# Optimization experiments

Hardware: AMD Instinct MI355X
Metric: run time of the kernel (lower is better)

## Reference

```python
import jax, jax.numpy as jnp
import numpy as np


def _cost_volume(x, y, maxdisp):
    # x, y: [N, C, H, W] left/right feature maps.
    # Replicates the torch loop:
    #   for i in range(D): d = D-1-i
    #     cost[:, :C, d, :, i:W]  = x[:, :, :, i:W]
    #     cost[:, C:, d, :, i:]   = y_pad[:, :, :, :W+D-i]   (y zero-padded to W+D)
    # =>  cost_x[d, j] = x[..., j]      if D-1-d <= j < W   else 0
    #     cost_y[d, j] = y[..., j-(D-1-d)] if 0 <= j-(D-1-d) < W else 0
    N, C, H, W = x.shape
    D = maxdisp
    Wc = W + D
    d = jnp.arange(D)
    i = (D - 1) - d                      # shift per depth plane, [D]
    j = jnp.arange(Wc)                   # output width coords, [Wc]

    # left-image half: same columns, masked per depth plane
    xp = jnp.pad(x, ((0, 0), (0, 0), (0, 0), (0, D)))          # [N,C,H,Wc]
    mask_x = (j[None, :] >= i[:, None]) & (j[None, :] < W)      # [D,Wc]
    cost_x = xp[:, :, None, :, :] * mask_x[None, None, :, None, :].astype(x.dtype)

    # right-image half: shifted gather with zero fill
    jy = j[None, :] - i[:, None]                                # [D,Wc]
    valid = (jy >= 0) & (jy < W)
    idx = jnp.clip(jy, 0, W - 1)
    y_g = y[:, :, :, idx]                                       # [N,C,H,D,Wc]
    cost_y = jnp.where(valid[None, None, None, :, :], y_g, jnp.zeros((), x.dtype))
    cost_y = cost_y.transpose(0, 1, 3, 2, 4)                    # [N,C,D,H,Wc]

    return jnp.concatenate([cost_x, cost_y], axis=1)            # [N,2C,D,H,Wc]


def setup_inputs() -> dict:
    key = jax.random.key(0)
    k1, k2 = jax.random.split(key)
    N, C, H, W = 2, 32, 64, 128
    x = jax.random.normal(k1, (N, C, H, W), dtype=jnp.float32)
    y = jax.random.normal(k2, (N, C, H, W), dtype=jnp.float32)
    return {"x": x, "y": y, "maxdisp": 48}


def reference(x, y, maxdisp):
    return _cost_volume(x, y, maxdisp)
```

## Files before the change

kernel.cpp:

```cpp
#include <hip/hip_runtime.h>

constexpr int N    = 2;
constexpr int C    = 32;
constexpr int H    = 64;
constexpr int W    = 128;
constexpr int D    = 48;
constexpr int Wc   = W + D;
constexpr int C2   = 2 * C;
constexpr int HWc  = H * Wc;
constexpr int Wc4  = Wc / 4;
constexpr int BQ   = D * Wc4;
constexpr int NBLOCKS = N * C2 * H;

typedef float vf4 __attribute__((ext_vector_type(4)));

__global__ __launch_bounds__(256)
void cost_volume_kernel(const float* __restrict__ x,
                        const float* __restrict__ y,
                        float* __restrict__ out)
{
    __shared__ __align__(16) float row[224];

    unsigned b   = blockIdx.x;
    unsigned tid = threadIdx.x;

    unsigned h  = b % H;
    unsigned t  = b / H;
    unsigned cc = t % C2;
    unsigned n  = t / C2;
    bool is_x = cc < C;

    if (is_x) {
        if (tid < 128)
            row[tid] = x[((n * C + cc) * H + h) * W + tid];
        else if (tid < 224)
            row[tid] = 0.0f;
    } else {
        if (tid < 48)
            row[tid] = 0.0f;
        else if (tid < 176)
            row[tid] = y[((n * C + (cc - C)) * H + h) * W + (tid - 48)];
        else if (tid < 224)
            row[tid] = 0.0f;
    }
    __syncthreads();

    vf4* __restrict__ outv = reinterpret_cast<vf4*>(out)
                           + (size_t)t * (D * (HWc / 4)) + h * Wc4;
    const vf4* __restrict__ rowv = reinterpret_cast<const vf4*>(row);

    if (is_x) {
        #pragma unroll
        for (int it = 0; it < 9; ++it) {
            unsigned q = tid + 256u * it;
            if (q >= (unsigned)BQ) break;
            unsigned d = q / 44u;
            unsigned v = q - 44u * d;
            int i  = (int)(47u - d);
            int j0 = 4 * (int)v;
            vf4 ld = rowv[v];
            vf4 o;
            o.x = (j0 + 0 >= i) ? ld.x : 0.0f;
            o.y = (j0 + 1 >= i) ? ld.y : 0.0f;
            o.z = (j0 + 2 >= i) ? ld.z : 0.0f;
            o.w = (j0 + 3 >= i) ? ld.w : 0.0f;
            outv[d * (unsigned)(HWc / 4) + v] = o;
        }
    } else {
        #pragma unroll
        for (int it = 0; it < 9; ++it) {
            unsigned q = tid + 256u * it;
            if (q >= (unsigned)BQ) break;
            unsigned d = q / 44u;
            unsigned v = q - 44u * d;
            int i = (int)(47u - d);
            int s = 48 + 4 * (int)v - i;
            vf4 o;
            o.x = row[s + 0];
            o.y = row[s + 1];
            o.z = row[s + 2];
            o.w = row[s + 3];
            outv[d * (unsigned)(HWc / 4) + v] = o;
        }
    }
}

extern "C" void kernel_launch(void* const* d_in, const int* in_sizes, int n_in,
                              void* d_out, int out_size, void* d_ws, size_t ws_size,
                              hipStream_t stream)
{
    const float* x = (const float*)d_in[0];
    const float* y = (const float*)d_in[1];
    float* out = (float*)d_out;

    cost_volume_kernel<<<dim3(NBLOCKS), dim3(256), 0, stream>>>(x, y, out);
}
```

Baseline: 299.2 us.

## Remap blocks to (n,c,d) planes and read inputs directly from global memory

Each block now writes one contiguous H×Wc depth plane instead of one row across all depth planes. The shared-memory staging and barrier are gone, and input values are read straight from global memory (cached in L1/L2) with clamped scalar loads for the shifted y half. Output stores use nontemporal hints to avoid polluting cache. This gives fully contiguous streaming writes per block, at the cost of redundant global reads of inputs across D blocks and four scalar loads per vector on the y side.

```diff
diff --git a/kernel.cpp b/kernel.cpp
--- a/kernel.cpp
+++ b/kernel.cpp
@@ -9,8 +9,8 @@
 constexpr int C2   = 2 * C;
 constexpr int HWc  = H * Wc;
 constexpr int Wc4  = Wc / 4;
-constexpr int BQ   = D * Wc4;
-constexpr int NBLOCKS = N * C2 * H;
+constexpr int PLANE_V4 = HWc / 4;
+constexpr int NBLOCKS  = N * C2 * D;
 
 typedef float vf4 __attribute__((ext_vector_type(4)));
 
@@ -19,68 +19,54 @@
                         const float* __restrict__ y,
                         float* __restrict__ out)
 {
-    __shared__ __align__(16) float row[224];
+    const unsigned b   = blockIdx.x;
+    const unsigned tid = threadIdx.x;
 
-    unsigned b   = blockIdx.x;
-    unsigned tid = threadIdx.x;
+    const unsigned d  = b % (unsigned)D;
+    const unsigned t  = b / (unsigned)D;
+    const unsigned cc = t % (unsigned)C2;
+    const unsigned n  = t / (unsigned)C2;
+    const int      i  = D - 1 - (int)d;
 
-    unsigned h  = b % H;
-    unsigned t  = b / H;
-    unsigned cc = t % C2;
-    unsigned n  = t / C2;
-    bool is_x = cc < C;
+    vf4* __restrict__ outv = reinterpret_cast<vf4*>(out) + (size_t)b * PLANE_V4;
 
-    if (is_x) {
-        if (tid < 128)
-            row[tid] = x[((n * C + cc) * H + h) * W + tid];
-        else if (tid < 224)
-            row[tid] = 0.0f;
-    } else {
-        if (tid < 48)
-            row[tid] = 0.0f;
-        else if (tid < 176)
-            row[tid] = y[((n * C + (cc - C)) * H + h) * W + (tid - 48)];
-        else if (tid < 224)
-            row[tid] = 0.0f;
-    }
-    __syncthreads();
-
-    vf4* __restrict__ outv = reinterpret_cast<vf4*>(out)
-                           + (size_t)t * (D * (HWc / 4)) + h * Wc4;
-    const vf4* __restrict__ rowv = reinterpret_cast<const vf4*>(row);
-
-    if (is_x) {
+    if (cc < (unsigned)C) {
+        const vf4* __restrict__ xv =
+            reinterpret_cast<const vf4*>(x + (size_t)(n * C + cc) * (H * W));
         #pragma unroll
-        for (int it = 0; it < 9; ++it) {
-            unsigned q = tid + 256u * it;
-            if (q >= (unsigned)BQ) break;
-            unsigned d = q / 44u;
-            unsigned v = q - 44u * d;
-            int i  = (int)(47u - d);
-            int j0 = 4 * (int)v;
-            vf4 ld = rowv[v];
-            vf4 o;
-            o.x = (j0 + 0 >= i) ? ld.x : 0.0f;
-            o.y = (j0 + 1 >= i) ? ld.y : 0.0f;
-            o.z = (j0 + 2 >= i) ? ld.z : 0.0f;
-            o.w = (j0 + 3 >= i) ? ld.w : 0.0f;
-            outv[d * (unsigned)(HWc / 4) + v] = o;
+        for (int it = 0; it < 11; ++it) {
+            unsigned q = tid + 256u * (unsigned)it;
+            unsigned h = q / 44u;
+            unsigned v = q - 44u * h;
+            vf4 o = (vf4){0.0f, 0.0f, 0.0f, 0.0f};
+            if (v < 32u) {
+                int j0 = 4 * (int)v;
+                vf4 ld = xv[h * 32u + v];
+                o.x = (j0 + 0 >= i) ? ld.x : 0.0f;
+                o.y = (j0 + 1 >= i) ? ld.y : 0.0f;
+                o.z = (j0 + 2 >= i) ? ld.z : 0.0f;
+                o.w = (j0 + 3 >= i) ? ld.w : 0.0f;
+            }
+            __builtin_nontemporal_store(o, &outv[q]);
         }
     } else {
+        const float* __restrict__ yp = y + (size_t)(n * C + (cc - C)) * (H * W);
         #pragma unroll
-        for (int it = 0; it < 9; ++it) {
-            unsigned q = tid + 256u * it;
-            if (q >= (unsigned)BQ) break;
-            unsigned d = q / 44u;
-            unsigned v = q - 44u * d;
-            int i = (int)(47u - d);
-            int s = 48 + 4 * (int)v - i;
+        for (int it = 0; it < 11; ++it) {
+            unsigned q = tid + 256u * (unsigned)it;
+            unsigned h = q / 44u;
+            unsigned v = q - 44u * h;
+            const float* __restrict__ yr = yp + h * (unsigned)W;
+            int s0 = 4 * (int)v - i;
             vf4 o;
-            o.x = row[s + 0];
-            o.y = row[s + 1];
-            o.z = row[s + 2];
-            o.w = row[s + 3];
-            outv[d * (unsigned)(HWc / 4) + v] = o;
+            #pragma unroll
+            for (int e = 0; e < 4; ++e) {
+                int s  = s0 + e;
+                int sc = s < 0 ? 0 : (s > W - 1 ? W - 1 : s);
+                float val = yr[sc];
+                o[e] = ((unsigned)s < (unsigned)W) ? val : 0.0f;
+            }
+            __builtin_nontemporal_store(o, &outv[q]);
         }
     }
 }
```

Measured after the change: 322.3 us. 1.08x slower.
